# Optimization experiments

Measured on AMD Instinct MI355X. Metric: run time of the kernel, lower is better.

The kernel has to match this reference:

```python
import jax, jax.numpy as jnp
import numpy as np

EMBED_DIM = 1024
HEAD_SIZE = 64
B, T = 4, 4096


def setup_inputs() -> dict:
    key = jax.random.key(0)
    kx, kq, kk, kv = jax.random.split(key, 4)
    x = jax.random.normal(kx, (B, T, EMBED_DIM), dtype=jnp.float32)
    sw = 1.0 / np.sqrt(EMBED_DIM)  # kaiming-ish init scale for linear weights
    Wq = jax.random.normal(kq, (EMBED_DIM, HEAD_SIZE), dtype=jnp.float32) * sw
    Wk = jax.random.normal(kk, (EMBED_DIM, HEAD_SIZE), dtype=jnp.float32) * sw
    Wv = jax.random.normal(kv, (EMBED_DIM, HEAD_SIZE), dtype=jnp.float32) * sw
    return {"x": x, "Wq": Wq, "Wk": Wk, "Wv": Wv}


def reference(x, Wq, Wk, Wv):
    Bn, Tn, C = x.shape
    q = jnp.einsum('btc,ch->bth', x, Wq)
    k = jnp.einsum('btc,ch->bth', x, Wk)
    v = jnp.einsum('btc,ch->bth', x, Wv)
    # NOTE: original scales by sqrt(C) = sqrt(embed_dim), not sqrt(head_size)
    scale = 1.0 / jnp.sqrt(jnp.asarray(C, dtype=x.dtype))
    wei = jnp.einsum('bth,bsh->bts', q, k) * scale  # [B, T, T]
    causal = jnp.tril(jnp.ones((Tn, Tn), dtype=bool))
    wei = jnp.where(causal, wei, -jnp.inf)
    wei = jax.nn.softmax(wei, axis=-1)
    # dropout p=0.0 (eval mode): identity
    return jnp.einsum('bts,bsh->bth', wei, v)
```

## Files before the change

### kernel.cpp

```cpp
#include <hip/hip_runtime.h>
#include <cstdint>


typedef __bf16 bf16;
typedef __bf16 bf16x8 __attribute__((ext_vector_type(8)));
typedef float  f32x4  __attribute__((ext_vector_type(4)));

#define MFMA16(a, b, c) __builtin_amdgcn_mfma_f32_16x16x32_bf16((a), (b), (c), 0, 0, 0)

#if __has_builtin(__builtin_amdgcn_exp2f)
#define EXP2(x) __builtin_amdgcn_exp2f(x)
#else
#define EXP2(x) exp2f(x)
#endif

#define B_SZ 4
#define T_SZ 4096
#define C_SZ 1024
#define H_SZ 64
#define M_SZ (B_SZ * T_SZ)
#define QSCALE (1.4426950408889634f / 32.0f)
#define P_STR 4160

__device__ __forceinline__ void dma16(const void* g, void* l) {
    __builtin_amdgcn_global_load_lds(
        (const __attribute__((address_space(1))) uint32_t*)(uintptr_t)g,
        (__attribute__((address_space(3))) uint32_t*)(uint32_t)(uintptr_t)l,
        16, 0, 0);
}

__global__ __launch_bounds__(256) void wt_prep(
    const float* __restrict__ Wq, const float* __restrict__ Wk,
    const float* __restrict__ Wv, bf16* __restrict__ wt2)
{
    const int n4 = blockIdx.x, t = threadIdx.x;
    const int nbase = n4 * 4;
    const float* W = (nbase < 64) ? Wq : (nbase < 128 ? Wk : Wv);
    const float sc = (nbase < 64) ? QSCALE : 1.0f;
    const int ncol = nbase & 63;
    #pragma unroll
    for (int i = 0; i < 4; ++i) {
        const int k = i * 256 + t;
        const float4 v = *(const float4*)(W + (size_t)k * H_SZ + ncol);
        const float vals[4] = {v.x, v.y, v.z, v.w};
        const size_t base = (size_t)(k >> 6) * 12288 + (size_t)((k >> 5) & 1) * 6144
                          + (size_t)((k >> 3) & 3) * 1536 + (k & 7);
        #pragma unroll
        for (int m = 0; m < 4; ++m)
            wt2[base + (size_t)(nbase + m) * 8] = (bf16)(vals[m] * sc);
    }
}

__global__ __launch_bounds__(256) void qkv_proj(
    const float* __restrict__ x, const bf16* __restrict__ wt2,
    bf16* __restrict__ qw, bf16* __restrict__ kw2, bf16* __restrict__ vtw2)
{
    const int m0 = blockIdx.x * 16;
    const int tid = threadIdx.x;
    const int wave = tid >> 6, lane = tid & 63;
    const int quad = lane >> 4, l15 = lane & 15;

    __shared__ __align__(16) float xs[2 * 4 * 16 * 8];
    __shared__ __align__(16) bf16  ws[2 * 4 * 192 * 8];

    f32x4 acc[3] = {};

    const char* xg = (const char*)x
        + (size_t)(m0 + ((tid >> 1) & 15)) * 4096
        + (size_t)(tid >> 7) * 128 + (size_t)((tid >> 5) & 3) * 32 + (size_t)(tid & 1) * 16;
    char* xl = (char*)xs + (size_t)tid * 16;
    const char* wg = (const char*)wt2 + (size_t)tid * 16;
    char* wl = (char*)ws + (size_t)tid * 16;

    for (int s = 0; s < 16; ++s) {
        __syncthreads();
        dma16(xg + (size_t)s * 256, xl);
        #pragma unroll
        for (int i = 0; i < 6; ++i)
            dma16(wg + (size_t)s * 24576 + (size_t)i * 4096, wl + (size_t)i * 4096);
        __syncthreads();

        #pragma unroll
        for (int ss = 0; ss < 2; ++ss) {
            bf16x8 a;
            {
                const float* ap = xs + ss * 512 + quad * 128 + l15 * 8;
                const f32x4 lo = *(const f32x4*)ap;
                const f32x4 hi = *(const f32x4*)(ap + 4);
                a[0] = (bf16)lo[0]; a[1] = (bf16)lo[1];
                a[2] = (bf16)lo[2]; a[3] = (bf16)lo[3];
                a[4] = (bf16)hi[0]; a[5] = (bf16)hi[1];
                a[6] = (bf16)hi[2]; a[7] = (bf16)hi[3];
            }
            #pragma unroll
            for (int i = 0; i < 3; ++i) {
                const int nt = wave * 3 + i;
                const bf16x8 wf = *(const bf16x8*)(ws + ss * 6144 + quad * 1536
                                                   + (nt * 16 + l15) * 8);
                acc[i] = MFMA16(a, wf, acc[i]);
            }
        }
    }

    #pragma unroll
    for (int i = 0; i < 3; ++i) {
        const int n = (wave * 3 + i) * 16 + l15;
        const int which = n >> 6, col = n & 63;
        #pragma unroll
        for (int r = 0; r < 4; ++r) {
            const int t = m0 + quad * 4 + r;
            const bf16 v = (bf16)acc[i][r];
            if (which == 0) {
                qw[(size_t)t * H_SZ + col] = v;
            } else if (which == 1) {
                kw2[(size_t)(t >> 6) * 4096
                    + (size_t)(((col >> 5) << 2) + ((col >> 3) & 3)) * 512
                    + (size_t)(t & 63) * 8 + (col & 7)] = v;
            } else {
                vtw2[(size_t)(t >> 6) * 4096
                     + (size_t)((((t >> 5) & 1) << 2) + ((t >> 3) & 3)) * 512
                     + (size_t)col * 8 + (t & 7)] = v;
            }
        }
    }
}

__global__ __launch_bounds__(256) void flash_attn(
    const bf16* __restrict__ qw, const bf16* __restrict__ kw2,
    const bf16* __restrict__ vtw2, float* __restrict__ pbuf)
{
    const int bx = blockIdx.x;
    const int item = (bx & 1) ? (1023 - (bx >> 1)) : (bx >> 1);
    const int qt = 63 - (item >> 4);
    const int b  = (item >> 2) & 3;
    const int h  = item & 3;
    const int i0 = qt * 64;
    const int nkv = qt + 1;

    const int tid = threadIdx.x;
    const int mg = tid >> 6, lane = tid & 63;
    const int quad = lane >> 4, l15 = lane & 15;

    __shared__ __align__(16) bf16 kvs[8192];
    __shared__ __align__(16) bf16 pls[4][16 * 72];

    bf16x8 aq0, aq1;
    {
        const bf16* qp = qw + ((size_t)b * T_SZ + i0 + mg * 16 + l15) * H_SZ + quad * 8;
        aq0 = *(const bf16x8*)qp;
        aq1 = *(const bf16x8*)(qp + 32);
    }
    const bf16 onev = (bf16)1.0f;
    const bf16x8 vone = {onev, onev, onev, onev, onev, onev, onev, onev};

    const char* kgb = (const char*)kw2 + (size_t)b * 524288;
    const char* vgb = (const char*)vtw2 + (size_t)b * 524288;
    const bf16* kb = kvs;
    const bf16* vb = kvs + 4096;
    bf16* pl = pls[mg];

    f32x4 o[4] = {};
    f32x4 osum = {};

    for (int jt = h; jt < nkv; jt += 4) {
        __syncthreads();
        {
            const char* ks = kgb + (size_t)jt * 8192;
            const char* vs = vgb + (size_t)jt * 8192;
            char* dst = (char*)kvs + (size_t)tid * 16;
            dma16(ks + (size_t)tid * 16, dst);
            dma16(ks + 4096 + (size_t)tid * 16, dst + 4096);
            dma16(vs + (size_t)tid * 16, dst + 8192);
            dma16(vs + 4096 + (size_t)tid * 16, dst + 12288);
        }
        __syncthreads();

        f32x4 s4[4] = {};
        #pragma unroll
        for (int ct = 0; ct < 4; ++ct) {
            const bf16x8 k0 = *(const bf16x8*)(kb + (0 * 4 + quad) * 512 + (ct * 16 + l15) * 8);
            const bf16x8 k1 = *(const bf16x8*)(kb + (1 * 4 + quad) * 512 + (ct * 16 + l15) * 8);
            s4[ct] = MFMA16(aq0, k0, s4[ct]);
            s4[ct] = MFMA16(aq1, k1, s4[ct]);
        }
        if (jt == qt) {
            #pragma unroll
            for (int ct = 0; ct < 4; ++ct) {
                const int col = ct * 16 + l15;
                const int row = mg * 16 + quad * 4;
                #pragma unroll
                for (int rr = 0; rr < 4; ++rr)
                    if (col > row + rr) s4[ct][rr] = -3.0e38f;
            }
        }
        #pragma unroll
        for (int ct = 0; ct < 4; ++ct)
            #pragma unroll
            for (int rr = 0; rr < 4; ++rr)
                pl[(quad * 4 + rr) * 72 + ct * 16 + l15] = (bf16)EXP2(s4[ct][rr]);
        const bf16x8 pa0 = *(const bf16x8*)&pl[l15 * 72 + quad * 8];
        const bf16x8 pa1 = *(const bf16x8*)&pl[l15 * 72 + 32 + quad * 8];

        #pragma unroll
        for (int ht = 0; ht < 4; ++ht) {
            const bf16x8 v0 = *(const bf16x8*)(vb + (0 * 4 + quad) * 512 + (ht * 16 + l15) * 8);
            const bf16x8 v1 = *(const bf16x8*)(vb + (1 * 4 + quad) * 512 + (ht * 16 + l15) * 8);
            o[ht] = MFMA16(pa0, v0, o[ht]);
            o[ht] = MFMA16(pa1, v1, o[ht]);
        }
        osum = MFMA16(pa0, vone, osum);
        osum = MFMA16(pa1, vone, osum);
    }

    float* pb = pbuf + (size_t)(((b * 64 + qt) * 4) + h) * P_STR;
    #pragma unroll
    for (int ht = 0; ht < 4; ++ht)
        #pragma unroll
        for (int rr = 0; rr < 4; ++rr)
            pb[(mg * 16 + quad * 4 + rr) * 64 + ht * 16 + l15] = o[ht][rr];
    if (l15 == 0) {
        #pragma unroll
        for (int rr = 0; rr < 4; ++rr)
            pb[4096 + mg * 16 + quad * 4 + rr] = osum[rr];
    }
}

__global__ __launch_bounds__(256) void combine(
    const float* __restrict__ pbuf, float* __restrict__ out)
{
    const int bq = blockIdx.x, tid = threadIdx.x;
    const int row = tid >> 2, c0 = (tid & 3) * 16;
    const float* p = pbuf + (size_t)bq * 4 * P_STR;

    f32x4 a0 = {}, a1 = {}, a2 = {}, a3 = {};
    float l = 0.f;
    #pragma unroll
    for (int h = 0; h < 4; ++h) {
        const float* ph = p + (size_t)h * P_STR + row * 64 + c0;
        a0 += *(const f32x4*)(ph);
        a1 += *(const f32x4*)(ph + 4);
        a2 += *(const f32x4*)(ph + 8);
        a3 += *(const f32x4*)(ph + 12);
        l  += p[(size_t)h * P_STR + 4096 + row];
    }
    const float inv = 1.0f / l;
    float* op = out + ((size_t)bq * 64 + row) * 64 + c0;
    *(f32x4*)(op)      = a0 * inv;
    *(f32x4*)(op + 4)  = a1 * inv;
    *(f32x4*)(op + 8)  = a2 * inv;
    *(f32x4*)(op + 12) = a3 * inv;
}

extern "C" void kernel_launch(void* const* d_in, const int* in_sizes, int n_in,
                              void* d_out, int out_size, void* d_ws, size_t ws_size,
                              hipStream_t stream) {
    const float* x  = (const float*)d_in[0];
    const float* Wq = (const float*)d_in[1];
    const float* Wk = (const float*)d_in[2];
    const float* Wv = (const float*)d_in[3];

    bf16* qw   = (bf16*)d_ws;
    bf16* kw2  = qw + (size_t)M_SZ * H_SZ;
    bf16* vtw2 = kw2 + (size_t)M_SZ * H_SZ;
    bf16* wt2  = vtw2 + (size_t)M_SZ * H_SZ;
    float* pbuf = (float*)(wt2 + 3 * 64 * 1024);
    float* out = (float*)d_out;

    wt_prep<<<48, 256, 0, stream>>>(Wq, Wk, Wv, wt2);
    qkv_proj<<<M_SZ / 16, 256, 0, stream>>>(x, wt2, qw, kw2, vtw2);
    flash_attn<<<1024, 256, 0, stream>>>(qw, kw2, vtw2, pbuf);
    combine<<<256, 256, 0, stream>>>(pbuf, out);
}
```

Before: 162.9 us.

## Double QKV projection row tile to 32 and stagger K-loop start per block

The QKV projection kernel now processes 32 rows per block instead of 16, so each weight tile loaded into shared memory feeds two MFMA row groups. This halves the weight traffic per output row and halves the grid size. Each block also starts its K-loop at a different offset (blockIdx mod 16), which spreads concurrent blocks across different weight slices and reduces contention on the same cache lines. The cost is more accumulator registers and fewer blocks, which can lower occupancy.

```diff
diff --git a/kernel.cpp b/kernel.cpp
--- a/kernel.cpp
+++ b/kernel.cpp
@@ -55,74 +55,82 @@
     const float* __restrict__ x, const bf16* __restrict__ wt2,
     bf16* __restrict__ qw, bf16* __restrict__ kw2, bf16* __restrict__ vtw2)
 {
-    const int m0 = blockIdx.x * 16;
+    const int m0 = blockIdx.x * 32;
     const int tid = threadIdx.x;
     const int wave = tid >> 6, lane = tid & 63;
     const int quad = lane >> 4, l15 = lane & 15;
-
-    __shared__ __align__(16) float xs[2 * 4 * 16 * 8];
+    const int phase = blockIdx.x & 15;
+
+    __shared__ __align__(16) float xs[2 * 4 * 32 * 8];
     __shared__ __align__(16) bf16  ws[2 * 4 * 192 * 8];
 
-    f32x4 acc[3] = {};
+    f32x4 acc[2][3] = {};
 
     const char* xg = (const char*)x
-        + (size_t)(m0 + ((tid >> 1) & 15)) * 4096
-        + (size_t)(tid >> 7) * 128 + (size_t)((tid >> 5) & 3) * 32 + (size_t)(tid & 1) * 16;
+        + (size_t)(m0 + ((tid >> 1) & 31)) * 4096
+        + (size_t)((tid >> 6) & 3) * 32 + (size_t)(tid & 1) * 16;
     char* xl = (char*)xs + (size_t)tid * 16;
     const char* wg = (const char*)wt2 + (size_t)tid * 16;
     char* wl = (char*)ws + (size_t)tid * 16;
 
     for (int s = 0; s < 16; ++s) {
-        __syncthreads();
-        dma16(xg + (size_t)s * 256, xl);
+        const size_t se = (size_t)((s + phase) & 15);
+        __syncthreads();
+        dma16(xg + se * 256, xl);
+        dma16(xg + se * 256 + 128, xl + 4096);
         #pragma unroll
         for (int i = 0; i < 6; ++i)
-            dma16(wg + (size_t)s * 24576 + (size_t)i * 4096, wl + (size_t)i * 4096);
+            dma16(wg + se * 24576 + (size_t)i * 4096, wl + (size_t)i * 4096);
         __syncthreads();
 
         #pragma unroll
         for (int ss = 0; ss < 2; ++ss) {
-            bf16x8 a;
-            {
-                const float* ap = xs + ss * 512 + quad * 128 + l15 * 8;
+            bf16x8 a[2];
+            #pragma unroll
+            for (int mg = 0; mg < 2; ++mg) {
+                const float* ap = xs + ss * 1024 + quad * 256 + (mg * 16 + l15) * 8;
                 const f32x4 lo = *(const f32x4*)ap;
                 const f32x4 hi = *(const f32x4*)(ap + 4);
-                a[0] = (bf16)lo[0]; a[1] = (bf16)lo[1];
-                a[2] = (bf16)lo[2]; a[3] = (bf16)lo[3];
-                a[4] = (bf16)hi[0]; a[5] = (bf16)hi[1];
-                a[6] = (bf16)hi[2]; a[7] = (bf16)hi[3];
+                a[mg][0] = (bf16)lo[0]; a[mg][1] = (bf16)lo[1];
+                a[mg][2] = (bf16)lo[2]; a[mg][3] = (bf16)lo[3];
+                a[mg][4] = (bf16)hi[0]; a[mg][5] = (bf16)hi[1];
+                a[mg][6] = (bf16)hi[2]; a[mg][7] = (bf16)hi[3];
             }
             #pragma unroll
             for (int i = 0; i < 3; ++i) {
                 const int nt = wave * 3 + i;
                 const bf16x8 wf = *(const bf16x8*)(ws + ss * 6144 + quad * 1536
                                                    + (nt * 16 + l15) * 8);
-                acc[i] = MFMA16(a, wf, acc[i]);
-            }
-        }
-    }
-
-    #pragma unroll
-    for (int i = 0; i < 3; ++i) {
-        const int n = (wave * 3 + i) * 16 + l15;
-        const int which = n >> 6, col = n & 63;
-        #pragma unroll
-        for (int r = 0; r < 4; ++r) {
-            const int t = m0 + quad * 4 + r;
-            const bf16 v = (bf16)acc[i][r];
-            if (which == 0) {
-                qw[(size_t)t * H_SZ + col] = v;
-            } else if (which == 1) {
-                kw2[(size_t)(t >> 6) * 4096
-                    + (size_t)(((col >> 5) << 2) + ((col >> 3) & 3)) * 512
-                    + (size_t)(t & 63) * 8 + (col & 7)] = v;
-            } else {
-                vtw2[(size_t)(t >> 6) * 4096
-                     + (size_t)((((t >> 5) & 1) << 2) + ((t >> 3) & 3)) * 512
-                     + (size_t)col * 8 + (t & 7)] = v;
-            }
-        }
-    }
+                #pragma unroll
+                for (int mg = 0; mg < 2; ++mg)
+                    acc[mg][i] = MFMA16(a[mg], wf, acc[mg][i]);
+            }
+        }
+    }
+
+    #pragma unroll
+    for (int mg = 0; mg < 2; ++mg)
+        #pragma unroll
+        for (int i = 0; i < 3; ++i) {
+            const int n = (wave * 3 + i) * 16 + l15;
+            const int which = n >> 6, col = n & 63;
+            #pragma unroll
+            for (int r = 0; r < 4; ++r) {
+                const int t = m0 + mg * 16 + quad * 4 + r;
+                const bf16 v = (bf16)acc[mg][i][r];
+                if (which == 0) {
+                    qw[(size_t)t * H_SZ + col] = v;
+                } else if (which == 1) {
+                    kw2[(size_t)(t >> 6) * 4096
+                        + (size_t)(((col >> 5) << 2) + ((col >> 3) & 3)) * 512
+                        + (size_t)(t & 63) * 8 + (col & 7)] = v;
+                } else {
+                    vtw2[(size_t)(t >> 6) * 4096
+                         + (size_t)((((t >> 5) & 1) << 2) + ((t >> 3) & 3)) * 512
+                         + (size_t)col * 8 + (t & 7)] = v;
+                }
+            }
+        }
 }
 
 __global__ __launch_bounds__(256) void flash_attn(
@@ -267,7 +275,7 @@
     float* out = (float*)d_out;
 
     wt_prep<<<48, 256, 0, stream>>>(Wq, Wk, Wv, wt2);
-    qkv_proj<<<M_SZ / 16, 256, 0, stream>>>(x, wt2, qw, kw2, vtw2);
+    qkv_proj<<<M_SZ / 32, 256, 0, stream>>>(x, wt2, qw, kw2, vtw2);
     flash_attn<<<1024, 256, 0, stream>>>(qw, kw2, vtw2, pbuf);
     combine<<<256, 256, 0, stream>>>(pbuf, out);
 }
```

After: 151.1 us. 1.08x faster.

## Double-buffer KV and x tiles; read projection weights directly from global memory

Applied to the files above, without the earlier changes.

In flash_attn, K/V tiles are double-buffered in LDS so the DMA for the next tile is issued before computing on the current one, removing one barrier per iteration. In qkv_proj, the x tile is double-buffered over 8 larger k-steps, with a per-block phase offset that staggers accesses. Weight fragments are now read straight from a padded, transposed global weight layout instead of being staged through LDS. wt_prep is rewritten to produce that layout through an LDS transpose. This trades LDS traffic and barriers for more L2/global weight reads and higher LDS use in flash_attn, which may lower occupancy.

```diff
diff --git a/kernel.cpp b/kernel.cpp
--- a/kernel.cpp
+++ b/kernel.cpp
@@ -4,6 +4,7 @@
 
 typedef __bf16 bf16;
 typedef __bf16 bf16x8 __attribute__((ext_vector_type(8)));
+typedef __bf16 bf16x4 __attribute__((ext_vector_type(4)));
 typedef float  f32x4  __attribute__((ext_vector_type(4)));
 
 #define MFMA16(a, b, c) __builtin_amdgcn_mfma_f32_16x16x32_bf16((a), (b), (c), 0, 0, 0)
@@ -21,6 +22,8 @@
 #define M_SZ (B_SZ * T_SZ)
 #define QSCALE (1.4426950408889634f / 32.0f)
 #define P_STR 4160
+#define WT_STR 1088
+#define WT_SZ  (H_SZ * WT_STR)
 
 __device__ __forceinline__ void dma16(const void* g, void* l) {
     __builtin_amdgcn_global_load_lds(
@@ -31,60 +34,81 @@
 
 __global__ __launch_bounds__(256) void wt_prep(
     const float* __restrict__ Wq, const float* __restrict__ Wk,
-    const float* __restrict__ Wv, bf16* __restrict__ wt2)
+    const float* __restrict__ Wv, bf16* __restrict__ wt)
 {
-    const int n4 = blockIdx.x, t = threadIdx.x;
-    const int nbase = n4 * 4;
-    const float* W = (nbase < 64) ? Wq : (nbase < 128 ? Wk : Wv);
-    const float sc = (nbase < 64) ? QSCALE : 1.0f;
-    const int ncol = nbase & 63;
-    #pragma unroll
-    for (int i = 0; i < 4; ++i) {
-        const int k = i * 256 + t;
-        const float4 v = *(const float4*)(W + (size_t)k * H_SZ + ncol);
-        const float vals[4] = {v.x, v.y, v.z, v.w};
-        const size_t base = (size_t)(k >> 6) * 12288 + (size_t)((k >> 5) & 1) * 6144
-                          + (size_t)((k >> 3) & 3) * 1536 + (k & 7);
-        #pragma unroll
-        for (int m = 0; m < 4; ++m)
-            wt2[base + (size_t)(nbase + m) * 8] = (bf16)(vals[m] * sc);
-    }
+    const int which = blockIdx.x >> 4, kt = blockIdx.x & 15;
+    const float* W = (which == 0) ? Wq : ((which == 1) ? Wk : Wv);
+    const float s = (which == 0) ? QSCALE : 1.0f;
+    const int t = threadIdx.x;
+
+    __shared__ bf16 tile[64][72];
+
+    #pragma unroll
+    for (int j = 0; j < 4; ++j) {
+        const int f4 = t + j * 256;
+        const int kl = f4 >> 4, n4 = f4 & 15;
+        const float4 v = *(const float4*)(W + (size_t)(kt * 64 + kl) * H_SZ + n4 * 4);
+        tile[n4 * 4 + 0][kl] = (bf16)(v.x * s);
+        tile[n4 * 4 + 1][kl] = (bf16)(v.y * s);
+        tile[n4 * 4 + 2][kl] = (bf16)(v.z * s);
+        tile[n4 * 4 + 3][kl] = (bf16)(v.w * s);
+    }
+    __syncthreads();
+    const int n = t >> 2, kk = (t & 3) * 16;
+    bf16* dst = wt + (size_t)which * WT_SZ + (size_t)n * WT_STR + kt * 64 + kk;
+    *(bf16x8*)dst       = *(const bf16x8*)&tile[n][kk];
+    *(bf16x8*)(dst + 8) = *(const bf16x8*)&tile[n][kk + 8];
 }
 
 __global__ __launch_bounds__(256) void qkv_proj(
-    const float* __restrict__ x, const bf16* __restrict__ wt2,
+    const float* __restrict__ x, const bf16* __restrict__ wt,
     bf16* __restrict__ qw, bf16* __restrict__ kw2, bf16* __restrict__ vtw2)
 {
     const int m0 = blockIdx.x * 16;
     const int tid = threadIdx.x;
     const int wave = tid >> 6, lane = tid & 63;
     const int quad = lane >> 4, l15 = lane & 15;
-
-    __shared__ __align__(16) float xs[2 * 4 * 16 * 8];
-    __shared__ __align__(16) bf16  ws[2 * 4 * 192 * 8];
+    const int phase = blockIdx.x & 7;
+
+    __shared__ __align__(16) float xs[2][2048];
 
     f32x4 acc[3] = {};
 
     const char* xg = (const char*)x
         + (size_t)(m0 + ((tid >> 1) & 15)) * 4096
-        + (size_t)(tid >> 7) * 128 + (size_t)((tid >> 5) & 3) * 32 + (size_t)(tid & 1) * 16;
-    char* xl = (char*)xs + (size_t)tid * 16;
-    const char* wg = (const char*)wt2 + (size_t)tid * 16;
-    char* wl = (char*)ws + (size_t)tid * 16;
-
-    for (int s = 0; s < 16; ++s) {
+        + (size_t)((tid >> 7) & 1) * 128 + (size_t)((tid >> 5) & 3) * 32
+        + (size_t)(tid & 1) * 16;
+    char* xl = (char*)&xs[0][0] + (size_t)tid * 16;
+
+    const bf16* wpb[3];
+    #pragma unroll
+    for (int i = 0; i < 3; ++i) {
+        const int n = (wave * 3 + i) * 16 + l15;
+        wpb[i] = wt + (size_t)(n >> 6) * WT_SZ + (size_t)(n & 63) * WT_STR;
+    }
+
+    {
+        const size_t kb = (size_t)phase * 512;
+        dma16(xg + kb, xl);
+        dma16(xg + kb + 256, xl + 4096);
+    }
+
+    for (int s = 0; s < 8; ++s) {
+        const int slot = s & 1;
         __syncthreads();
-        dma16(xg + (size_t)s * 256, xl);
-        #pragma unroll
-        for (int i = 0; i < 6; ++i)
-            dma16(wg + (size_t)s * 24576 + (size_t)i * 4096, wl + (size_t)i * 4096);
-        __syncthreads();
-
-        #pragma unroll
-        for (int ss = 0; ss < 2; ++ss) {
+        if (s + 1 < 8) {
+            const size_t kb = (size_t)(((s + 1) + phase) & 7) * 512;
+            char* nxt = (char*)&xs[slot ^ 1][0] + (size_t)tid * 16;
+            dma16(xg + kb, nxt);
+            dma16(xg + kb + 256, nxt + 4096);
+        }
+        const int se = (s + phase) & 7;
+
+        #pragma unroll
+        for (int ss = 0; ss < 4; ++ss) {
             bf16x8 a;
             {
-                const float* ap = xs + ss * 512 + quad * 128 + l15 * 8;
+                const float* ap = &xs[slot][((ss * 4 + quad) * 16 + l15) * 8];
                 const f32x4 lo = *(const f32x4*)ap;
                 const f32x4 hi = *(const f32x4*)(ap + 4);
                 a[0] = (bf16)lo[0]; a[1] = (bf16)lo[1];
@@ -92,11 +116,10 @@
                 a[4] = (bf16)hi[0]; a[5] = (bf16)hi[1];
                 a[6] = (bf16)hi[2]; a[7] = (bf16)hi[3];
             }
+            const int k = se * 128 + ss * 32 + quad * 8;
             #pragma unroll
             for (int i = 0; i < 3; ++i) {
-                const int nt = wave * 3 + i;
-                const bf16x8 wf = *(const bf16x8*)(ws + ss * 6144 + quad * 1536
-                                                   + (nt * 16 + l15) * 8);
+                const bf16x8 wf = *(const bf16x8*)(wpb[i] + k);
                 acc[i] = MFMA16(a, wf, acc[i]);
             }
         }
@@ -141,7 +164,7 @@
     const int mg = tid >> 6, lane = tid & 63;
     const int quad = lane >> 4, l15 = lane & 15;
 
-    __shared__ __align__(16) bf16 kvs[8192];
+    __shared__ __align__(16) bf16 kvs[2][8192];
     __shared__ __align__(16) bf16 pls[4][16 * 72];
 
     bf16x8 aq0, aq1;
@@ -155,25 +178,29 @@
 
     const char* kgb = (const char*)kw2 + (size_t)b * 524288;
     const char* vgb = (const char*)vtw2 + (size_t)b * 524288;
-    const bf16* kb = kvs;
-    const bf16* vb = kvs + 4096;
     bf16* pl = pls[mg];
 
     f32x4 o[4] = {};
     f32x4 osum = {};
 
-    for (int jt = h; jt < nkv; jt += 4) {
+    auto dmaKV = [&](int jt, int slot) {
+        const char* ks = kgb + (size_t)jt * 8192;
+        const char* vs = vgb + (size_t)jt * 8192;
+        char* dst = (char*)&kvs[slot][0] + (size_t)tid * 16;
+        dma16(ks + (size_t)tid * 16, dst);
+        dma16(ks + 4096 + (size_t)tid * 16, dst + 4096);
+        dma16(vs + (size_t)tid * 16, dst + 8192);
+        dma16(vs + 4096 + (size_t)tid * 16, dst + 12288);
+    };
+
+    if (h < nkv) dmaKV(h, 0);
+    int slot = 0;
+    for (int jt = h; jt < nkv; jt += 4, slot ^= 1) {
         __syncthreads();
-        {
-            const char* ks = kgb + (size_t)jt * 8192;
-            const char* vs = vgb + (size_t)jt * 8192;
-            char* dst = (char*)kvs + (size_t)tid * 16;
-            dma16(ks + (size_t)tid * 16, dst);
-            dma16(ks + 4096 + (size_t)tid * 16, dst + 4096);
-            dma16(vs + (size_t)tid * 16, dst + 8192);
-            dma16(vs + 4096 + (size_t)tid * 16, dst + 12288);
-        }
-        __syncthreads();
+        if (jt + 4 < nkv) dmaKV(jt + 4, slot ^ 1);
+
+        const bf16* kb = &kvs[slot][0];
+        const bf16* vb = kb + 4096;
 
         f32x4 s4[4] = {};
         #pragma unroll
@@ -262,12 +289,12 @@
     bf16* qw   = (bf16*)d_ws;
     bf16* kw2  = qw + (size_t)M_SZ * H_SZ;
     bf16* vtw2 = kw2 + (size_t)M_SZ * H_SZ;
-    bf16* wt2  = vtw2 + (size_t)M_SZ * H_SZ;
-    float* pbuf = (float*)(wt2 + 3 * 64 * 1024);
+    bf16* wt   = vtw2 + (size_t)M_SZ * H_SZ;
+    float* pbuf = (float*)(wt + 3 * WT_SZ);
     float* out = (float*)d_out;
 
-    wt_prep<<<48, 256, 0, stream>>>(Wq, Wk, Wv, wt2);
-    qkv_proj<<<M_SZ / 16, 256, 0, stream>>>(x, wt2, qw, kw2, vtw2);
+    wt_prep<<<48, 256, 0, stream>>>(Wq, Wk, Wv, wt);
+    qkv_proj<<<M_SZ / 16, 256, 0, stream>>>(x, wt, qw, kw2, vtw2);
     flash_attn<<<1024, 256, 0, stream>>>(qw, kw2, vtw2, pbuf);
     combine<<<256, 256, 0, stream>>>(pbuf, out);
 }
```

Result: slower. 175.2 us (+7.5%).
